# Kernel optimization log

Hardware: AMD Instinct MI355X
Metric: run time of the kernel (lower is better)

The kernel has to match this reference:

```python
import jax, jax.numpy as jnp
import numpy as np

N = 200000   # atoms
M = 12       # neighbors per atom
F = 64       # atom_fea_len
NBR = 41     # nbr_fea_len
ORIG = 92    # orig_atom_fea_len
B = 2000     # crystals
SH = 9       # dim of 0e+1o+2e spherical harmonics (lmax=2)
NCONV = 3
HFEA = 128


def _sph_harm_l2(v):
    # real spherical harmonics up to l=2 on normalized vectors ('integral' norm)
    r = jnp.sqrt(jnp.sum(v * v, axis=-1, keepdims=True))
    u = v / jnp.maximum(r, 1e-9)
    x, y, z = u[..., 0], u[..., 1], u[..., 2]
    c0 = 0.28209479177387814   # 1/(2*sqrt(pi))
    c1 = 0.4886025119029199    # sqrt(3/(4*pi))
    c2 = 1.0925484305920792
    return jnp.stack([
        jnp.full_like(x, c0),
        c1 * y, c1 * z, c1 * x,
        c2 * x * y, c2 * y * z,
        0.31539156525252005 * (3.0 * z * z - 1.0),
        c2 * x * z,
        0.5462742152960396 * (x * x - y * y),
    ], axis=-1)


def setup_inputs() -> dict:
    key = jax.random.key(0)
    ks = jax.random.split(key, 12)
    s = 0.05
    return {
        "atom_fea": jax.random.normal(ks[0], (N, ORIG), jnp.float32),
        "nbr_fea": jax.random.uniform(ks[1], (N, M, NBR), dtype=jnp.float32),
        "nbr_idx": jax.random.randint(ks[2], (N, M), 0, N),
        "crystal_atom_idx": jnp.arange(N).reshape(B, N // B),
        "pos": jax.random.normal(ks[3], (N, 3), jnp.float32),
        "W_emb": jax.random.normal(ks[4], (ORIG, F), jnp.float32) * s,
        "b_emb": jnp.zeros((F,), jnp.float32),
        "Wr1": jax.random.normal(ks[5], (NCONV, NBR, NBR), jnp.float32) * s,
        "br1": jnp.zeros((NCONV, NBR), jnp.float32),
        "Wr2": jax.random.normal(ks[6], (NCONV, NBR, SH), jnp.float32) * s,
        "br2": jnp.zeros((NCONV, SH), jnp.float32),
        "Wtp": jax.random.normal(ks[7], (NCONV, F, F), jnp.float32) * s,
        "W_fc": jax.random.normal(ks[8], (F, HFEA), jnp.float32) * s,
        "b_fc": jnp.zeros((HFEA,), jnp.float32),
        "W_out": jax.random.normal(ks[9], (HFEA, 1), jnp.float32) * s,
        "b_out": jnp.zeros((1,), jnp.float32),
    }


def reference(atom_fea, nbr_fea, nbr_idx, crystal_atom_idx, pos,
              W_emb, b_emb, Wr1, br1, Wr2, br2, Wtp, W_fc, b_fc, W_out, b_out):
    x = atom_fea @ W_emb + b_emb                       # [N, F]
    src = nbr_idx.reshape(-1)                          # [N*M]
    e = nbr_fea.reshape(N * M, NBR)
    # dst = arange(N) repeated M times -> pos[dst] is just pos repeated
    rel = pos[src] - jnp.repeat(pos, M, axis=0)        # [N*M, 3]
    Y = _sph_harm_l2(rel)                              # [N*M, 9]
    Y0 = Y[:, :1]                                      # only 0e path feeds the TP output
    alpha = 1.0 / jnp.sqrt(jnp.float32(F))             # e3nn path normalization
    for l in range(NCONV):
        R = jax.nn.softplus(e @ Wr1[l] + br1[l]) @ Wr2[l] + br2[l]   # [N*M, 9]
        W0 = R[:, :1] * Y0                                           # scalar gate per edge
        msg = (x[src] @ Wtp[l]) * W0 * alpha                          # [N*M, F]
        # scatter-mean over dst == mean over the fixed M neighbors
        x = msg.reshape(N, M, F).mean(axis=1)
    crys = x[crystal_atom_idx].mean(axis=1)            # [B, F]
    h = jax.nn.softplus(crys @ W_fc + b_fc)            # [B, HFEA]
    out = h @ W_out + b_out                            # [B, 1]
    return (out, h)
```

## Files before the change

kernel.cpp:

```cpp
#include <hip/hip_runtime.h>
#include <hip/hip_bf16.h>
#include <math.h>

#define N_ATOMS 200000
#define M_NBR 12
#define F_DIM 64
#define NBR_FEA 41
#define ORIG_F 92
#define B_CRYS 2000
#define APB 100
#define SH_DIM 9
#define NCONV 3
#define HFEA 128
#define EDGES (N_ATOMS * M_NBR)

typedef __attribute__((ext_vector_type(8))) short short8;
typedef __attribute__((ext_vector_type(4))) float floatx4;

__device__ __forceinline__ float softplus_f(float x) {
    return fmaxf(x, 0.0f) + __logf(1.0f + __expf(-fabsf(x)));
}
__device__ __forceinline__ unsigned short f2bf(float f) {
    __hip_bfloat16 h = __float2bfloat16(f);
    return *reinterpret_cast<unsigned short*>(&h);
}
__device__ __forceinline__ float bf2f(unsigned int u) {
    unsigned int x = u << 16;
    union { unsigned int i; float f; } c; c.i = x; return c.f;
}

__global__ __launch_bounds__(256) void k_embed(
    const float* __restrict__ atom_fea, const float* __restrict__ W_emb,
    const float* __restrict__ b_emb, unsigned short* __restrict__ x)
{
    __shared__ float ldsW[ORIG_F * F_DIM];
    __shared__ float ldsA[16 * ORIG_F];
    int tid = threadIdx.x;
    for (int i = tid; i < ORIG_F * F_DIM; i += 256) ldsW[i] = W_emb[i];
    long base = (long)blockIdx.x * 16;
    for (int i = tid; i < 16 * ORIG_F; i += 256) ldsA[i] = atom_fea[base * ORIG_F + i];
    __syncthreads();
    int col = tid & 63;
    int rg  = tid >> 6;
    float a0 = 0.f, a1 = 0.f, a2 = 0.f, a3 = 0.f;
    const float* Ar = &ldsA[(rg * 4) * ORIG_F];
    for (int k = 0; k < ORIG_F; ++k) {
        float wv = ldsW[k * F_DIM + col];
        a0 = fmaf(Ar[0 * ORIG_F + k], wv, a0);
        a1 = fmaf(Ar[1 * ORIG_F + k], wv, a1);
        a2 = fmaf(Ar[2 * ORIG_F + k], wv, a2);
        a3 = fmaf(Ar[3 * ORIG_F + k], wv, a3);
    }
    float bb = b_emb[col];
    long o = (base + rg * 4) * F_DIM + col;
    x[o]             = f2bf(a0 + bb);
    x[o + F_DIM]     = f2bf(a1 + bb);
    x[o + 2 * F_DIM] = f2bf(a2 + bb);
    x[o + 3 * F_DIM] = f2bf(a3 + bb);
}

__global__ __launch_bounds__(256) void k_filter(
    const float* __restrict__ nbr_fea, const float* __restrict__ Wr1,
    const float* __restrict__ br1, const float* __restrict__ Wr2,
    const float* __restrict__ br2, float* __restrict__ W0)
{
    __shared__ __align__(16) unsigned short ldsA[256 * 72];
    __shared__ __align__(16) unsigned short ldsWt[48 * 72];
    __shared__ float ldsw2[48];
    __shared__ float ldsb1[48];

    int tid  = threadIdx.x;
    int lane = tid & 63;
    int wv   = tid >> 6;
    int sub  = lane & 15;
    int quad = lane >> 4;
    long ebase = (long)blockIdx.x * 256;

    {
        short8 z = {0,0,0,0,0,0,0,0};
        for (int i = tid * 8; i < 256 * 72; i += 256 * 8)
            *(short8*)&ldsA[i] = z;
    }
    __syncthreads();
    {
        const float4* src4 = (const float4*)(nbr_fea + ebase * NBR_FEA);
        for (int i = tid; i < 2624; i += 256) {
            float4 v = src4[i];
            int b = i * 4;
            int i0 = b,     r0 = i0 / 41, c0 = i0 - r0 * 41;
            int i1 = b + 1, r1 = i1 / 41, c1 = i1 - r1 * 41;
            int i2 = b + 2, r2 = i2 / 41, c2 = i2 - r2 * 41;
            int i3 = b + 3, r3 = i3 / 41, c3 = i3 - r3 * 41;
            ldsA[r0 * 72 + c0] = f2bf(v.x);
            ldsA[r1 * 72 + c1] = f2bf(v.y);
            ldsA[r2 * 72 + c2] = f2bf(v.z);
            ldsA[r3 * 72 + c3] = f2bf(v.w);
        }
    }

    for (int l = 0; l < NCONV; ++l) {
        __syncthreads();
        for (int i = tid; i < 48 * 72; i += 256) {
            int n = i / 72, k = i - n * 72;
            unsigned short val = 0;
            if (n < NBR_FEA && k < NBR_FEA)
                val = f2bf(Wr1[l * NBR_FEA * NBR_FEA + k * NBR_FEA + n]);
            ldsWt[i] = val;
        }
        if (tid < 48) {
            ldsw2[tid] = (tid < NBR_FEA) ? Wr2[(l * NBR_FEA + tid) * SH_DIM] : 0.f;
            ldsb1[tid] = (tid < NBR_FEA) ? br1[l * NBR_FEA + tid] : 0.f;
        }
        __syncthreads();

        floatx4 acc[4][3];
        #pragma unroll
        for (int mt = 0; mt < 4; ++mt)
            #pragma unroll
            for (int nt = 0; nt < 3; ++nt)
                acc[mt][nt] = (floatx4){0.f, 0.f, 0.f, 0.f};

        #pragma unroll
        for (int s = 0; s < 2; ++s) {
            int koff = s * 32 + quad * 8;
            short8 bfr[3];
            #pragma unroll
            for (int nt = 0; nt < 3; ++nt)
                bfr[nt] = *(const short8*)&ldsWt[(nt * 16 + sub) * 72 + koff];
            #pragma unroll
            for (int mt = 0; mt < 4; ++mt) {
                short8 afr = *(const short8*)&ldsA[(wv * 64 + mt * 16 + sub) * 72 + koff];
                #pragma unroll
                for (int nt = 0; nt < 3; ++nt)
                    acc[mt][nt] = __builtin_amdgcn_mfma_f32_16x16x32_bf16(
                        afr, bfr[nt], acc[mt][nt], 0, 0, 0);
            }
        }

        float w2v[3], b1v[3];
        #pragma unroll
        for (int nt = 0; nt < 3; ++nt) {
            w2v[nt] = ldsw2[nt * 16 + sub];
            b1v[nt] = ldsb1[nt * 16 + sub];
        }
        float r2b = br2[l * SH_DIM];
        #pragma unroll
        for (int mt = 0; mt < 4; ++mt) {
            float p[4];
            #pragma unroll
            for (int reg = 0; reg < 4; ++reg) {
                float t = 0.f;
                #pragma unroll
                for (int nt = 0; nt < 3; ++nt)
                    t += softplus_f(acc[mt][nt][reg] + b1v[nt]) * w2v[nt];
                t += __shfl_xor(t, 1);
                t += __shfl_xor(t, 2);
                t += __shfl_xor(t, 4);
                t += __shfl_xor(t, 8);
                p[reg] = t + r2b;
            }
            if (sub == 0) {
                long base = (long)l * EDGES + ebase + wv * 64 + mt * 16 + quad * 4;
                W0[base + 0] = p[0];
                W0[base + 1] = p[1];
                W0[base + 2] = p[2];
                W0[base + 3] = p[3];
            }
        }
    }
}

__global__ __launch_bounds__(256) void k_conv(
    const unsigned short* __restrict__ x_in, const int* __restrict__ nbr_idx,
    const float* __restrict__ W0, const float* __restrict__ Wtp,
    unsigned short* __restrict__ x_out)
{
    __shared__ float g[16][F_DIM];
    int tid  = threadIdx.x;
    int lane = tid & 63;
    int wv   = tid >> 6;
    int aw   = lane >> 4;
    int fq   = lane & 15;
    const float cscale = 0.28209479177387814f * 0.125f / 12.0f;

    long atom = (long)blockIdx.x * 16 + wv * 4 + aw;
    long eb = atom * M_NBR;
    float4 acc = {0.f, 0.f, 0.f, 0.f};
    #pragma unroll
    for (int j = 0; j < M_NBR; ++j) {
        int   idx = nbr_idx[eb + j];
        float wj  = W0[eb + j];
        uint2 v = *(const uint2*)(x_in + (size_t)idx * F_DIM + fq * 4);
        acc.x = fmaf(wj, bf2f(v.x & 0xffffu), acc.x);
        acc.y = fmaf(wj, bf2f(v.x >> 16),     acc.y);
        acc.z = fmaf(wj, bf2f(v.y & 0xffffu), acc.z);
        acc.w = fmaf(wj, bf2f(v.y >> 16),     acc.w);
    }
    float4 gv = {acc.x * cscale, acc.y * cscale, acc.z * cscale, acc.w * cscale};
    *(float4*)&g[wv * 4 + aw][fq * 4] = gv;
    __syncthreads();

    int f = lane;
    float o0 = 0.f, o1 = 0.f, o2 = 0.f, o3 = 0.f;
    int r0 = wv * 4;
    for (int k4 = 0; k4 < F_DIM; k4 += 4) {
        float4 ga = *(const float4*)&g[r0 + 0][k4];
        float4 gb = *(const float4*)&g[r0 + 1][k4];
        float4 gc = *(const float4*)&g[r0 + 2][k4];
        float4 gd = *(const float4*)&g[r0 + 3][k4];
        #pragma unroll
        for (int t = 0; t < 4; ++t) {
            float wtv = Wtp[(k4 + t) * F_DIM + f];
            float gaa = (t == 0) ? ga.x : (t == 1) ? ga.y : (t == 2) ? ga.z : ga.w;
            float gbb = (t == 0) ? gb.x : (t == 1) ? gb.y : (t == 2) ? gb.z : gb.w;
            float gcc = (t == 0) ? gc.x : (t == 1) ? gc.y : (t == 2) ? gc.z : gc.w;
            float gdd = (t == 0) ? gd.x : (t == 1) ? gd.y : (t == 2) ? gd.z : gd.w;
            o0 = fmaf(gaa, wtv, o0);
            o1 = fmaf(gbb, wtv, o1);
            o2 = fmaf(gcc, wtv, o2);
            o3 = fmaf(gdd, wtv, o3);
        }
    }
    size_t ob = ((size_t)blockIdx.x * 16 + r0) * F_DIM + f;
    x_out[ob]             = f2bf(o0);
    x_out[ob + F_DIM]     = f2bf(o1);
    x_out[ob + 2 * F_DIM] = f2bf(o2);
    x_out[ob + 3 * F_DIM] = f2bf(o3);
}

__global__ __launch_bounds__(128) void k_readout(
    const unsigned short* __restrict__ x, const int* __restrict__ cidx,
    const float* __restrict__ W_fc, const float* __restrict__ b_fc,
    const float* __restrict__ W_out, const float* __restrict__ b_out,
    float* __restrict__ out, float* __restrict__ hout)
{
    __shared__ float part[2][F_DIM];
    __shared__ float crys[F_DIM];
    __shared__ float hw[HFEA];
    int tid = threadIdx.x;
    int c = blockIdx.x;
    int f = tid & 63, half = tid >> 6;
    const int* ci = cidx + c * APB + half * (APB / 2);
    float p = 0.f;
    for (int a = 0; a < APB / 2; ++a)
        p += bf2f(x[(size_t)ci[a] * F_DIM + f]);
    part[half][f] = p;
    __syncthreads();
    if (tid < F_DIM) crys[tid] = (part[0][tid] + part[1][tid]) * (1.0f / APB);
    __syncthreads();
    float acc = b_fc[tid];
    for (int ff = 0; ff < F_DIM; ++ff)
        acc = fmaf(crys[ff], W_fc[ff * HFEA + tid], acc);
    float h = softplus_f(acc);
    hout[(size_t)c * HFEA + tid] = h;
    hw[tid] = h * W_out[tid];
    __syncthreads();
    if (tid == 0) {
        float s = b_out[0];
        #pragma unroll 16
        for (int j = 0; j < HFEA; ++j) s += hw[j];
        out[c] = s;
    }
}

extern "C" void kernel_launch(void* const* d_in, const int* in_sizes, int n_in,
                              void* d_out, int out_size, void* d_ws, size_t ws_size,
                              hipStream_t stream) {
    const float* atom_fea = (const float*)d_in[0];
    const float* nbr_fea  = (const float*)d_in[1];
    const int*   nbr_idx  = (const int*)d_in[2];
    const int*   cidx     = (const int*)d_in[3];
    const float* W_emb = (const float*)d_in[5];
    const float* b_emb = (const float*)d_in[6];
    const float* Wr1   = (const float*)d_in[7];
    const float* br1   = (const float*)d_in[8];
    const float* Wr2   = (const float*)d_in[9];
    const float* br2   = (const float*)d_in[10];
    const float* Wtp   = (const float*)d_in[11];
    const float* W_fc  = (const float*)d_in[12];
    const float* b_fc  = (const float*)d_in[13];
    const float* W_out = (const float*)d_in[14];
    const float* b_out = (const float*)d_in[15];

    float* out  = (float*)d_out;
    float* hout = out + B_CRYS;

    float* W0 = (float*)d_ws;
    unsigned short* xA = (unsigned short*)(W0 + 3 * (size_t)EDGES);
    unsigned short* xB = xA + (size_t)N_ATOMS * F_DIM;

    k_embed <<<N_ATOMS / 16, 256, 0, stream>>>(atom_fea, W_emb, b_emb, xA);
    k_filter<<<EDGES / 256, 256, 0, stream>>>(nbr_fea, Wr1, br1, Wr2, br2, W0);
    k_conv  <<<N_ATOMS / 16, 256, 0, stream>>>(xA, nbr_idx, W0,             Wtp,                     xB);
    k_conv  <<<N_ATOMS / 16, 256, 0, stream>>>(xB, nbr_idx, W0 + EDGES,     Wtp + F_DIM * F_DIM,     xA);
    k_conv  <<<N_ATOMS / 16, 256, 0, stream>>>(xA, nbr_idx, W0 + 2 * EDGES, Wtp + 2 * F_DIM * F_DIM, xB);
    k_readout<<<B_CRYS, 128, 0, stream>>>(xB, cidx, W_fc, b_fc, W_out, b_out, out, hout);
}
```

Measured before the change: 1.138 ms.

## Load filter MFMA fragments directly from global and prepack weights

The filter kernel no longer stages nbr_fea and Wr1 through shared memory. Each lane loads its A-fragment rows straight from global memory into registers. The weights are prepacked once by a new single-block kernel into a per-lane bf16 fragment layout, together with padded w2/b1 vectors, so each filter block skips the per-layer transpose, the barriers and the LDS zeroing. The W0 stores are also vectorised. The trade-off is uncoalesced, unaligned row loads (41-float stride) in place of coalesced float4 loads, plus one extra tiny launch. The packed weights live in the xB buffer, which is only overwritten later.

```diff
diff --git a/kernel.cpp b/kernel.cpp
--- a/kernel.cpp
+++ b/kernel.cpp
@@ -17,6 +17,8 @@
 typedef __attribute__((ext_vector_type(8))) short short8;
 typedef __attribute__((ext_vector_type(4))) float floatx4;
 
+struct f4u { float x, y, z, w; };
+
 __device__ __forceinline__ float softplus_f(float x) {
     return fmaxf(x, 0.0f) + __logf(1.0f + __expf(-fabsf(x)));
 }
@@ -59,16 +61,41 @@
     x[o + 3 * F_DIM] = f2bf(a3 + bb);
 }
 
+__global__ __launch_bounds__(256) void k_prep(
+    const float* __restrict__ Wr1, const float* __restrict__ br1,
+    const float* __restrict__ Wr2, unsigned short* __restrict__ wpak,
+    float* __restrict__ w2p, float* __restrict__ b1p)
+{
+    int t = threadIdx.x;
+    for (int i = t; i < 64 * 18 * 8; i += 256) {
+        int lane = i / 144;
+        int rem  = i - lane * 144;
+        int fid  = rem >> 3;
+        int j    = rem & 7;
+        int l  = fid / 6;
+        int rf = fid - l * 6;
+        int nt = rf >> 1;
+        int s  = rf & 1;
+        int n = nt * 16 + (lane & 15);
+        int k = s * 32 + (lane >> 4) * 8 + j;
+        unsigned short v = 0;
+        if (n < NBR_FEA && k < NBR_FEA)
+            v = f2bf(Wr1[(l * NBR_FEA + k) * NBR_FEA + n]);
+        wpak[i] = v;
+    }
+    for (int i = t; i < 3 * 48; i += 256) {
+        int l = i / 48, n = i - l * 48;
+        w2p[i] = (n < NBR_FEA) ? Wr2[(l * NBR_FEA + n) * SH_DIM] : 0.f;
+        b1p[i] = (n < NBR_FEA) ? br1[l * NBR_FEA + n] : 0.f;
+    }
+}
+
 __global__ __launch_bounds__(256) void k_filter(
-    const float* __restrict__ nbr_fea, const float* __restrict__ Wr1,
-    const float* __restrict__ br1, const float* __restrict__ Wr2,
+    const float* __restrict__ nbr_fea,
+    const unsigned short* __restrict__ wpak,
+    const float* __restrict__ w2p, const float* __restrict__ b1p,
     const float* __restrict__ br2, float* __restrict__ W0)
 {
-    __shared__ __align__(16) unsigned short ldsA[256 * 72];
-    __shared__ __align__(16) unsigned short ldsWt[48 * 72];
-    __shared__ float ldsw2[48];
-    __shared__ float ldsb1[48];
-
     int tid  = threadIdx.x;
     int lane = tid & 63;
     int wv   = tid >> 6;
@@ -76,42 +103,43 @@
     int quad = lane >> 4;
     long ebase = (long)blockIdx.x * 256;
 
-    {
-        short8 z = {0,0,0,0,0,0,0,0};
-        for (int i = tid * 8; i < 256 * 72; i += 256 * 8)
-            *(short8*)&ldsA[i] = z;
-    }
-    __syncthreads();
-    {
-        const float4* src4 = (const float4*)(nbr_fea + ebase * NBR_FEA);
-        for (int i = tid; i < 2624; i += 256) {
-            float4 v = src4[i];
-            int b = i * 4;
-            int i0 = b,     r0 = i0 / 41, c0 = i0 - r0 * 41;
-            int i1 = b + 1, r1 = i1 / 41, c1 = i1 - r1 * 41;
-            int i2 = b + 2, r2 = i2 / 41, c2 = i2 - r2 * 41;
-            int i3 = b + 3, r3 = i3 / 41, c3 = i3 - r3 * 41;
-            ldsA[r0 * 72 + c0] = f2bf(v.x);
-            ldsA[r1 * 72 + c1] = f2bf(v.y);
-            ldsA[r2 * 72 + c2] = f2bf(v.z);
-            ldsA[r3 * 72 + c3] = f2bf(v.w);
+    short8 afr[4][2];
+    #pragma unroll
+    for (int mt = 0; mt < 4; ++mt) {
+        long r = ebase + wv * 64 + mt * 16 + sub;
+        const float* rowp = nbr_fea + r * NBR_FEA;
+        f4u a = *(const f4u*)(rowp + quad * 8);
+        f4u b = *(const f4u*)(rowp + quad * 8 + 4);
+        short8 f0;
+        f0[0] = (short)f2bf(a.x); f0[1] = (short)f2bf(a.y);
+        f0[2] = (short)f2bf(a.z); f0[3] = (short)f2bf(a.w);
+        f0[4] = (short)f2bf(b.x); f0[5] = (short)f2bf(b.y);
+        f0[6] = (short)f2bf(b.z); f0[7] = (short)f2bf(b.w);
+        afr[mt][0] = f0;
+        short8 f1 = {0, 0, 0, 0, 0, 0, 0, 0};
+        if (quad == 0) {
+            f4u c = *(const f4u*)(rowp + 32);
+            f4u d = *(const f4u*)(rowp + 36);
+            f1[0] = (short)f2bf(c.x); f1[1] = (short)f2bf(c.y);
+            f1[2] = (short)f2bf(c.z); f1[3] = (short)f2bf(c.w);
+            f1[4] = (short)f2bf(d.x); f1[5] = (short)f2bf(d.y);
+            f1[6] = (short)f2bf(d.z); f1[7] = (short)f2bf(d.w);
+        } else if (quad == 1) {
+            f1[0] = (short)f2bf(rowp[40]);
         }
-    }
-
+        afr[mt][1] = f1;
+    }
+
+    const unsigned short* bbase = wpak + lane * 144;
+
+    #pragma unroll
     for (int l = 0; l < NCONV; ++l) {
-        __syncthreads();
-        for (int i = tid; i < 48 * 72; i += 256) {
-            int n = i / 72, k = i - n * 72;
-            unsigned short val = 0;
-            if (n < NBR_FEA && k < NBR_FEA)
-                val = f2bf(Wr1[l * NBR_FEA * NBR_FEA + k * NBR_FEA + n]);
-            ldsWt[i] = val;
-        }
-        if (tid < 48) {
-            ldsw2[tid] = (tid < NBR_FEA) ? Wr2[(l * NBR_FEA + tid) * SH_DIM] : 0.f;
-            ldsb1[tid] = (tid < NBR_FEA) ? br1[l * NBR_FEA + tid] : 0.f;
-        }
-        __syncthreads();
+        short8 bfr[3][2];
+        #pragma unroll
+        for (int nt = 0; nt < 3; ++nt)
+            #pragma unroll
+            for (int s = 0; s < 2; ++s)
+                bfr[nt][s] = *(const short8*)(bbase + ((l * 3 + nt) * 2 + s) * 8);
 
         floatx4 acc[4][3];
         #pragma unroll
@@ -121,27 +149,19 @@
                 acc[mt][nt] = (floatx4){0.f, 0.f, 0.f, 0.f};
 
         #pragma unroll
-        for (int s = 0; s < 2; ++s) {
-            int koff = s * 32 + quad * 8;
-            short8 bfr[3];
+        for (int s = 0; s < 2; ++s)
             #pragma unroll
-            for (int nt = 0; nt < 3; ++nt)
-                bfr[nt] = *(const short8*)&ldsWt[(nt * 16 + sub) * 72 + koff];
-            #pragma unroll
-            for (int mt = 0; mt < 4; ++mt) {
-                short8 afr = *(const short8*)&ldsA[(wv * 64 + mt * 16 + sub) * 72 + koff];
+            for (int mt = 0; mt < 4; ++mt)
                 #pragma unroll
                 for (int nt = 0; nt < 3; ++nt)
                     acc[mt][nt] = __builtin_amdgcn_mfma_f32_16x16x32_bf16(
-                        afr, bfr[nt], acc[mt][nt], 0, 0, 0);
-            }
-        }
+                        afr[mt][s], bfr[nt][s], acc[mt][nt], 0, 0, 0);
 
         float w2v[3], b1v[3];
         #pragma unroll
         for (int nt = 0; nt < 3; ++nt) {
-            w2v[nt] = ldsw2[nt * 16 + sub];
-            b1v[nt] = ldsb1[nt * 16 + sub];
+            w2v[nt] = w2p[l * 48 + nt * 16 + sub];
+            b1v[nt] = b1p[l * 48 + nt * 16 + sub];
         }
         float r2b = br2[l * SH_DIM];
         #pragma unroll
@@ -161,10 +181,7 @@
             }
             if (sub == 0) {
                 long base = (long)l * EDGES + ebase + wv * 64 + mt * 16 + quad * 4;
-                W0[base + 0] = p[0];
-                W0[base + 1] = p[1];
-                W0[base + 2] = p[2];
-                W0[base + 3] = p[3];
+                *(floatx4*)&W0[base] = (floatx4){p[0], p[1], p[2], p[3]};
             }
         }
     }
@@ -289,8 +306,13 @@
     unsigned short* xA = (unsigned short*)(W0 + 3 * (size_t)EDGES);
     unsigned short* xB = xA + (size_t)N_ATOMS * F_DIM;
 
+    unsigned short* wpak = xB;
+    float* w2p = (float*)(wpak + 64 * 18 * 8);
+    float* b1p = w2p + 3 * 48;
+
+    k_prep  <<<1, 256, 0, stream>>>(Wr1, br1, Wr2, wpak, w2p, b1p);
     k_embed <<<N_ATOMS / 16, 256, 0, stream>>>(atom_fea, W_emb, b_emb, xA);
-    k_filter<<<EDGES / 256, 256, 0, stream>>>(nbr_fea, Wr1, br1, Wr2, br2, W0);
+    k_filter<<<EDGES / 256, 256, 0, stream>>>(nbr_fea, wpak, w2p, b1p, br2, W0);
     k_conv  <<<N_ATOMS / 16, 256, 0, stream>>>(xA, nbr_idx, W0,             Wtp,                     xB);
     k_conv  <<<N_ATOMS / 16, 256, 0, stream>>>(xB, nbr_idx, W0 + EDGES,     Wtp + F_DIM * F_DIM,     xA);
     k_conv  <<<N_ATOMS / 16, 256, 0, stream>>>(xA, nbr_idx, W0 + 2 * EDGES, Wtp + 2 * F_DIM * F_DIM, xB);
```

New measurement: 983.8 us. -13.5%, faster.
